# Kernel optimization log

Measured on AMD Instinct MI355X. Metric: run time of the kernel, lower is better.

## Reference

```python
import jax, jax.numpy as jnp
import numpy as np

N, E, H = 100000, 3200000, 128


def setup_inputs() -> dict:
    key = jax.random.key(0)
    ks = jax.random.split(key, 12)
    s = 1.0 / np.sqrt(H)
    x = jax.random.normal(ks[0], (N, H), dtype=jnp.float32)
    edge_index = jax.random.randint(ks[1], (2, E), 0, N, dtype=jnp.int64)
    # GatedGraphConv weight: [num_layers=1, H, H] -> single [H, H]
    W = jax.random.normal(ks[2], (H, H), dtype=jnp.float32) * s
    # GRUCell (gate order: r, z, n)
    gru_w_ih = jax.random.normal(ks[3], (3 * H, H), dtype=jnp.float32) * s
    gru_w_hh = jax.random.normal(ks[4], (3 * H, H), dtype=jnp.float32) * s
    gru_b_ih = jax.random.normal(ks[5], (3 * H,), dtype=jnp.float32) * s
    gru_b_hh = jax.random.normal(ks[6], (3 * H,), dtype=jnp.float32) * s
    # LSTM layer 0 (gate order: i, f, g, o)
    lstm_w_ih = jax.random.normal(ks[7], (4 * H, H), dtype=jnp.float32) * s
    lstm_w_hh = jax.random.normal(ks[8], (4 * H, H), dtype=jnp.float32) * s
    lstm_b_ih = jax.random.normal(ks[9], (4 * H,), dtype=jnp.float32) * s
    lstm_b_hh = jax.random.normal(ks[10], (4 * H,), dtype=jnp.float32) * s
    return {
        "x": x, "edge_index": edge_index, "W": W,
        "gru_w_ih": gru_w_ih, "gru_w_hh": gru_w_hh,
        "gru_b_ih": gru_b_ih, "gru_b_hh": gru_b_hh,
        "lstm_w_ih": lstm_w_ih, "lstm_w_hh": lstm_w_hh,
        "lstm_b_ih": lstm_b_ih, "lstm_b_hh": lstm_b_hh,
    }


def _forward(x, edge_index, W, gru_w_ih, gru_w_hh, gru_b_ih, gru_b_hh,
             lstm_w_ih, lstm_w_hh, lstm_b_ih, lstm_b_hh):
    n = x.shape[0]
    src, dst = edge_index[0], edge_index[1]
    # GatedGraphConv, num_layers=1, mean aggregation
    m = x @ W                                   # [N, H]
    msg = m[src]                                # [E, H] gather (memory-bound)
    agg_sum = jax.ops.segment_sum(msg, dst, num_segments=n)
    deg = jax.ops.segment_sum(jnp.ones((src.shape[0],), x.dtype), dst, num_segments=n)
    agg = agg_sum / jnp.maximum(deg, 1.0)[:, None]
    # GRUCell(agg, x): gates r, z, n
    gi = agg @ gru_w_ih.T + gru_b_ih
    gh = x @ gru_w_hh.T + gru_b_hh
    i_r, i_z, i_n = jnp.split(gi, 3, axis=-1)
    h_r, h_z, h_n = jnp.split(gh, 3, axis=-1)
    r = jax.nn.sigmoid(i_r + h_r)
    z = jax.nn.sigmoid(i_z + h_z)
    ng = jnp.tanh(i_n + r * h_n)
    h_conv = (1.0 - z) * ng + z * x             # conv output H_tilde
    # 1-layer LSTM over seq_len=1 with zero initial (H, C)
    gates = h_conv @ lstm_w_ih.T + lstm_b_ih + lstm_b_hh  # h0 = 0
    i_g, f_g, g_g, o_g = jnp.split(gates, 4, axis=-1)
    c = jax.nn.sigmoid(i_g) * jnp.tanh(g_g)
    h_lstm = jax.nn.sigmoid(o_g) * jnp.tanh(c)
    return jax.nn.relu(h_lstm)


def reference(x, edge_index, W, gru_w_ih, gru_w_hh, gru_b_ih, gru_b_hh,
              lstm_w_ih, lstm_w_hh, lstm_b_ih, lstm_b_hh):
    return _forward(x, edge_index, W, gru_w_ih, gru_w_hh, gru_b_ih, gru_b_hh,
                    lstm_w_ih, lstm_w_hh, lstm_b_ih, lstm_b_hh)
```

## Files before the change

### kernel.cpp

```cpp
#include <hip/hip_runtime.h>
#include <math.h>

#define HD 128
#define PB 256
#define SCB 4096

typedef __attribute__((ext_vector_type(8))) short short8;
typedef __attribute__((ext_vector_type(4))) float f32x4;
typedef __attribute__((ext_vector_type(2))) float f32x2;
typedef __attribute__((ext_vector_type(4))) unsigned u32x4;

__device__ __forceinline__ float sigf(float v) { return 1.0f / (1.0f + __expf(-v)); }
__device__ __forceinline__ float tanhf_fast(float v) {
  float e = __expf(2.0f * v);
  return 1.0f - 2.0f / (e + 1.0f);
}

__device__ __forceinline__ unsigned short f2bf(float f) {
  union { float f; unsigned u; } v; v.f = f;
  unsigned r = (v.u + 0x7fffu + ((v.u >> 16) & 1u)) >> 16;
  return (unsigned short)r;
}
__device__ __forceinline__ float bf2f(unsigned short b) {
  union { unsigned u; float f; } v; v.u = ((unsigned)b) << 16;
  return v.f;
}


__global__ __launch_bounds__(256) void bcount_k(const int* __restrict__ ei,
                                                int* __restrict__ bcnt,
                                                int E, int N, int shift, int NB) {
  __shared__ int h[256];
  const int blk = blockIdx.x, tid = threadIdx.x;
  h[tid] = 0;
  __syncthreads();
  int per = (E + PB - 1) / PB;
  int lo = blk * per;
  int hi = (lo + per < E) ? lo + per : E;
  for (int e = lo + tid; e < hi; e += 256) {
    int d = ei[(size_t)E + e];
    if ((unsigned)d >= (unsigned)N) continue;
    atomicAdd(&h[d >> shift], 1);
  }
  __syncthreads();
  if (tid < NB) bcnt[tid * PB + blk] = h[tid];
}

__global__ __launch_bounds__(256) void scan1_k(const int* __restrict__ a,
                                               int* __restrict__ bsums, int total) {
  __shared__ int ts[256];
  int b = blockIdx.x, tid = threadIdx.x;
  int lo = b * SCB + tid * 16;
  int s = 0;
#pragma unroll
  for (int i = 0; i < 16; ++i) {
    int idx = lo + i;
    if (idx < total) s += a[idx];
  }
  ts[tid] = s;
  __syncthreads();
  for (int off = 128; off > 0; off >>= 1) {
    if (tid < off) ts[tid] += ts[tid + off];
    __syncthreads();
  }
  if (tid == 0) bsums[b] = ts[0];
}

__global__ __launch_bounds__(256) void scan2_k(int* __restrict__ bsums, int nb) {
  __shared__ int ts[256];
  int tid = threadIdx.x;
  int v = (tid < nb) ? bsums[tid] : 0;
  ts[tid] = v;
  __syncthreads();
  for (int off = 1; off < 256; off <<= 1) {
    int u = (tid >= off) ? ts[tid - off] : 0;
    __syncthreads();
    ts[tid] += u;
    __syncthreads();
  }
  if (tid < nb) bsums[tid] = ts[tid] - v;
}

__global__ __launch_bounds__(256) void scan3_k(int* __restrict__ a,
                                               const int* __restrict__ bsums,
                                               int total, int nblk) {
  __shared__ int ts[256];
  int b = blockIdx.x, tid = threadIdx.x;
  int lo = b * SCB + tid * 16;
  int pre[16];
  int s = 0;
#pragma unroll
  for (int i = 0; i < 16; ++i) {
    int idx = lo + i;
    int xv = (idx < total) ? a[idx] : 0;
    pre[i] = s;
    s += xv;
  }
  ts[tid] = s;
  __syncthreads();
  for (int off = 1; off < 256; off <<= 1) {
    int u = (tid >= off) ? ts[tid - off] : 0;
    __syncthreads();
    ts[tid] += u;
    __syncthreads();
  }
  int off0 = ts[tid] - s + bsums[b];
#pragma unroll
  for (int i = 0; i < 16; ++i) {
    int idx = lo + i;
    if (idx < total) a[idx] = off0 + pre[i];
  }
  if (b == nblk - 1 && tid == 255) a[total] = off0 + s;
}

__global__ __launch_bounds__(256) void bpart_k(const int* __restrict__ ei,
                                               const int* __restrict__ bstart,
                                               unsigned* __restrict__ ebuf,
                                               int E, int N, int shift, int NB,
                                               int sbits) {
  __shared__ int cur[256];
  const int blk = blockIdx.x, tid = threadIdx.x;
  if (tid < NB) cur[tid] = bstart[tid * PB + blk];
  __syncthreads();
  int per = (E + PB - 1) / PB;
  int lo = blk * per;
  int hi = (lo + per < E) ? lo + per : E;
  const unsigned dmask = (1u << shift) - 1u;
  for (int e = lo + tid; e < hi; e += 256) {
    int s = ei[e];
    int d = ei[(size_t)E + e];
    if ((unsigned)s >= (unsigned)N || (unsigned)d >= (unsigned)N) continue;
    int p = atomicAdd(&cur[d >> shift], 1);
    ebuf[p] = (((unsigned)d & dmask) << sbits) | (unsigned)s;
  }
}

__global__ __launch_bounds__(256) void bfill2_k(const unsigned* __restrict__ ebuf,
                                                const int* __restrict__ bstart,
                                                int* __restrict__ rowstart,
                                                int* __restrict__ csr,
                                                int N, int shift, int NB, int sbits) {
  __shared__ int cnt[2048];
  __shared__ int tsum[256];
  const int b = blockIdx.x, tid = threadIdx.x;
  const int d0 = b << shift;
  int dmax = d0 + (1 << shift);
  if (dmax > N) dmax = N;
  const int nd = dmax - d0;
  const unsigned smask = (1u << sbits) - 1u;
  for (int i = tid; i < nd; i += 256) cnt[i] = 0;
  __syncthreads();
  const int base = bstart[b * PB];
  const int end = bstart[(b + 1) * PB];
  for (int idx = base + tid; idx < end; idx += 256)
    atomicAdd(&cnt[ebuf[idx] >> sbits], 1);
  __syncthreads();
  const int C = (nd + 255) / 256;
  int lo = tid * C;
  int hi = (lo + C < nd) ? lo + C : nd;
  int loc[8];
  int s = 0;
  for (int i = lo; i < hi; ++i) {
    loc[i - lo] = cnt[i];
    s += cnt[i];
  }
  tsum[tid] = s;
  __syncthreads();
  for (int off = 1; off < 256; off <<= 1) {
    int u = (tid >= off) ? tsum[tid - off] : 0;
    __syncthreads();
    tsum[tid] += u;
    __syncthreads();
  }
  int run = tsum[tid] - s + base;
  for (int i = lo; i < hi; ++i) {
    rowstart[d0 + i] = run;
    cnt[i] = run;
    run += loc[i - lo];
  }
  if (b == NB - 1 && tid == 255) rowstart[N] = end;
  __syncthreads();
  for (int idx = base + tid; idx < end; idx += 256) {
    unsigned pk = ebuf[idx];
    int p = atomicAdd(&cnt[pk >> sbits], 1);
    csr[p] = (int)(pk & smask);
  }
}


__global__ __launch_bounds__(256) void convx_k(const float* __restrict__ x,
                                               unsigned short* __restrict__ xb,
                                               unsigned* __restrict__ x8, int n4) {
  int t = blockIdx.x * 256 + threadIdx.x;
  if (t >= n4) return;
  float4 v = reinterpret_cast<const float4*>(x)[t];
  ushort4 o;
  o.x = f2bf(v.x); o.y = f2bf(v.y); o.z = f2bf(v.z); o.w = f2bf(v.w);
  reinterpret_cast<ushort4*>(xb)[t] = o;
  int p8 = 0;
  p8 = __builtin_amdgcn_cvt_pk_fp8_f32(v.x, v.y, p8, false);
  p8 = __builtin_amdgcn_cvt_pk_fp8_f32(v.z, v.w, p8, true);
  x8[t] = (unsigned)p8;
}

__global__ __launch_bounds__(256) void prepw_k(
    const float* __restrict__ gwhh, const float* __restrict__ lwih,
    const float* __restrict__ lbih, const float* __restrict__ lbhh,
    unsigned short* __restrict__ gwhhb, unsigned short* __restrict__ lwb,
    float* __restrict__ lbias) {
  int t = blockIdx.x * 256 + threadIdx.x;
  if (t < 49152) { gwhhb[t] = f2bf(gwhh[t]); return; }
  t -= 49152;
  if (t < 49152) {
    int j = t >> 7, k = t & 127;
    int jm = j < 128 ? j : j + 128;
    lwb[t] = f2bf(lwih[(size_t)jm * 128 + k]);
    return;
  }
  t -= 49152;
  if (t < 384) {
    int jm = t < 128 ? t : t + 128;
    lbias[t] = lbih[jm] + lbhh[jm];
  }
}

__global__ __launch_bounds__(256) void prepbp_k(const float* __restrict__ W,
                                                const float* __restrict__ gwih,
                                                unsigned short* __restrict__ Bpb) {
  int t = blockIdx.x * 256 + threadIdx.x;
  if (t >= 49152) return;
  int j = t >> 7, k = t & 127;
  const float4* wr = reinterpret_cast<const float4*>(W + (size_t)k * 128);
  const float4* gr = reinterpret_cast<const float4*>(gwih + (size_t)j * 128);
  float acc = 0.f;
#pragma unroll
  for (int c = 0; c < 32; ++c) {
    float4 a = wr[c], b = gr[c];
    acc += a.x * b.x + a.y * b.y + a.z * b.z + a.w * b.w;
  }
  Bpb[t] = f2bf(acc);
}

__device__ __forceinline__ void accf8(f32x2* acc, uint4 v) {
  acc[0] += __builtin_amdgcn_cvt_pk_f32_fp8((int)v.x, false);
  acc[1] += __builtin_amdgcn_cvt_pk_f32_fp8((int)v.x, true);
  acc[2] += __builtin_amdgcn_cvt_pk_f32_fp8((int)v.y, false);
  acc[3] += __builtin_amdgcn_cvt_pk_f32_fp8((int)v.y, true);
  acc[4] += __builtin_amdgcn_cvt_pk_f32_fp8((int)v.z, false);
  acc[5] += __builtin_amdgcn_cvt_pk_f32_fp8((int)v.z, true);
  acc[6] += __builtin_amdgcn_cvt_pk_f32_fp8((int)v.w, false);
  acc[7] += __builtin_amdgcn_cvt_pk_f32_fp8((int)v.w, true);
}

__global__ __launch_bounds__(256) void gather_f8_k(const int* __restrict__ csr,
                                                   const int* __restrict__ rowstart,
                                                   const unsigned* __restrict__ x8,
                                                   unsigned short* __restrict__ xaggb, int N) {
  int w = (int)(((long long)blockIdx.x * 256 + threadIdx.x) >> 6);
  if (w >= N) return;
  const int lane = threadIdx.x & 63;
  const int sub = lane >> 3, li = lane & 7;
  const int beg = rowstart[w], end = rowstart[w + 1];
  const uint4* x4 = reinterpret_cast<const uint4*>(x8);

  f32x2 acc[8];
#pragma unroll
  for (int i = 0; i < 8; ++i) acc[i] = (f32x2)0.f;

  int j = beg;
  for (; j + 32 <= end; j += 32) {
    int s0 = __builtin_nontemporal_load(&csr[j + sub]);
    int s1 = __builtin_nontemporal_load(&csr[j + 8 + sub]);
    int s2 = __builtin_nontemporal_load(&csr[j + 16 + sub]);
    int s3 = __builtin_nontemporal_load(&csr[j + 24 + sub]);
    uint4 v0 = x4[(size_t)s0 * 8 + li];
    uint4 v1 = x4[(size_t)s1 * 8 + li];
    uint4 v2 = x4[(size_t)s2 * 8 + li];
    uint4 v3 = x4[(size_t)s3 * 8 + li];
    accf8(acc, v0);
    accf8(acc, v1);
    accf8(acc, v2);
    accf8(acc, v3);
  }
  for (; j + 8 <= end; j += 8) {
    int s0 = __builtin_nontemporal_load(&csr[j + sub]);
    uint4 v0 = x4[(size_t)s0 * 8 + li];
    accf8(acc, v0);
  }
  int rem = end - j;
  if (sub < rem) {
    int s0 = csr[j + sub];
    uint4 v0 = x4[(size_t)s0 * 8 + li];
    accf8(acc, v0);
  }

  float a16[16];
#pragma unroll
  for (int i = 0; i < 8; ++i) { a16[2 * i] = acc[i].x; a16[2 * i + 1] = acc[i].y; }
#pragma unroll
  for (int i = 0; i < 16; ++i) {
    a16[i] += __shfl_xor(a16[i], 8, 64);
    a16[i] += __shfl_xor(a16[i], 16, 64);
    a16[i] += __shfl_xor(a16[i], 32, 64);
  }

  if (lane < 8) {
    float scale = 1.0f / fmaxf((float)(end - beg), 1.0f);
    u32x4 o1, o2;
    o1.x = (unsigned)f2bf(a16[0] * scale) | ((unsigned)f2bf(a16[1] * scale) << 16);
    o1.y = (unsigned)f2bf(a16[2] * scale) | ((unsigned)f2bf(a16[3] * scale) << 16);
    o1.z = (unsigned)f2bf(a16[4] * scale) | ((unsigned)f2bf(a16[5] * scale) << 16);
    o1.w = (unsigned)f2bf(a16[6] * scale) | ((unsigned)f2bf(a16[7] * scale) << 16);
    o2.x = (unsigned)f2bf(a16[8] * scale) | ((unsigned)f2bf(a16[9] * scale) << 16);
    o2.y = (unsigned)f2bf(a16[10] * scale) | ((unsigned)f2bf(a16[11] * scale) << 16);
    o2.z = (unsigned)f2bf(a16[12] * scale) | ((unsigned)f2bf(a16[13] * scale) << 16);
    o2.w = (unsigned)f2bf(a16[14] * scale) | ((unsigned)f2bf(a16[15] * scale) << 16);
    u32x4* dst = reinterpret_cast<u32x4*>(xaggb + (size_t)w * HD) + li * 2;
    __builtin_nontemporal_store(o1, dst);
    __builtin_nontemporal_store(o2, dst + 1);
  }
}

__global__ __launch_bounds__(256) void gru_fused_k(
    const unsigned short* __restrict__ xaggb, const unsigned short* __restrict__ xb,
    const unsigned short* __restrict__ Bpb, const unsigned short* __restrict__ gwhhb,
    const float* __restrict__ gbih, const float* __restrict__ gbhh,
    unsigned short* __restrict__ hconv, int nrows) {
  __shared__ unsigned short Bsm[6][32][136];
  const int tid = threadIdx.x;
  const int w = tid >> 6, lane = tid & 63;
  const int q = lane >> 4, r = lane & 15;
  const int row0 = blockIdx.y * 64;
  const int c0 = blockIdx.x * 32;

#pragma unroll
  for (int it = 0; it < 12; ++it) {
    int idx = it * 256 + tid;
    int p = idx >> 9;
    int rem = idx & 511;
    int col = rem >> 4, kq = rem & 15;
    const unsigned short* src =
        (p < 3) ? Bpb + ((size_t)(p * 128 + c0 + col)) * HD
                : gwhhb + ((size_t)((p - 3) * 128 + c0 + col)) * HD;
    uint4 v = *reinterpret_cast<const uint4*>(src + kq * 8);
    *reinterpret_cast<uint4*>(&Bsm[p][col][kq * 8]) = v;
  }
  __syncthreads();

  int arow = row0 + (w << 4) + r;
  int ar = arow < nrows ? arow : nrows - 1;
  const unsigned short* Aa = xaggb + (size_t)ar * HD + q * 8;
  const unsigned short* Ax = xb + (size_t)ar * HD + q * 8;

  f32x4 acc[6][2];
#pragma unroll
  for (int p = 0; p < 6; ++p)
#pragma unroll
    for (int cb = 0; cb < 2; ++cb) acc[p][cb] = (f32x4)0.f;

#pragma unroll
  for (int ks = 0; ks < 4; ++ks) {
    short8 a1 = *reinterpret_cast<const short8*>(Aa + ks * 32);
    short8 a2 = *reinterpret_cast<const short8*>(Ax + ks * 32);
#pragma unroll
    for (int p = 0; p < 6; ++p) {
      short8 af = (p < 3) ? a1 : a2;
#pragma unroll
      for (int cb = 0; cb < 2; ++cb) {
        short8 bf = *reinterpret_cast<const short8*>(&Bsm[p][cb * 16 + r][ks * 32 + q * 8]);
        acc[p][cb] = __builtin_amdgcn_mfma_f32_16x16x32_bf16(af, bf, acc[p][cb], 0, 0, 0);
      }
    }
  }

#pragma unroll
  for (int cb = 0; cb < 2; ++cb) {
    int col = c0 + cb * 16 + r;
    float bir = gbih[col], biz = gbih[col + 128], bin = gbih[col + 256];
    float bhr = gbhh[col], bhz = gbhh[col + 128], bhn = gbhh[col + 256];
#pragma unroll
    for (int reg = 0; reg < 4; ++reg) {
      int row = row0 + (w << 4) + q * 4 + reg;
      if (row < nrows) {
        float ir = acc[0][cb][reg] + bir, iz = acc[1][cb][reg] + biz;
        float inn = acc[2][cb][reg] + bin;
        float hr = acc[3][cb][reg] + bhr, hz = acc[4][cb][reg] + bhz;
        float hn = acc[5][cb][reg] + bhn;
        float rr = sigf(ir + hr), zz = sigf(iz + hz);
        float nn = tanhf_fast(inn + rr * hn);
        float xv = bf2f(xb[(size_t)row * HD + col]);
        hconv[(size_t)row * HD + col] = f2bf((1.f - zz) * nn + zz * xv);
      }
    }
  }
}

__global__ __launch_bounds__(256) void lstm_fused_k(
    const unsigned short* __restrict__ hconv, const unsigned short* __restrict__ lwb,
    const float* __restrict__ lbias, float* __restrict__ out, int nrows) {
  __shared__ unsigned short Bsm[3][64][136];
  const int tid = threadIdx.x;
  const int w = tid >> 6, lane = tid & 63;
  const int q = lane >> 4, r = lane & 15;
  const int row0 = blockIdx.y * 64;
  const int c0 = blockIdx.x * 64;

#pragma unroll
  for (int it = 0; it < 12; ++it) {
    int idx = it * 256 + tid;
    int p = idx >> 10, rem = idx & 1023;
    int col = rem >> 4, kq = rem & 15;
    uint4 v = *reinterpret_cast<const uint4*>(
        lwb + ((size_t)(p * 128 + c0 + col)) * HD + kq * 8);
    *reinterpret_cast<uint4*>(&Bsm[p][col][kq * 8]) = v;
  }
  __syncthreads();

  int arow = row0 + (w << 4) + r;
  int ar = arow < nrows ? arow : nrows - 1;
  const unsigned short* Ap = hconv + (size_t)ar * HD + q * 8;

  f32x4 acc[3][4];
#pragma unroll
  for (int p = 0; p < 3; ++p)
#pragma unroll
    for (int cb = 0; cb < 4; ++cb) acc[p][cb] = (f32x4)0.f;

#pragma unroll
  for (int ks = 0; ks < 4; ++ks) {
    short8 af = *reinterpret_cast<const short8*>(Ap + ks * 32);
#pragma unroll
    for (int p = 0; p < 3; ++p)
#pragma unroll
      for (int cb = 0; cb < 4; ++cb) {
        short8 bf = *reinterpret_cast<const short8*>(&Bsm[p][cb * 16 + r][ks * 32 + q * 8]);
        acc[p][cb] = __builtin_amdgcn_mfma_f32_16x16x32_bf16(af, bf, acc[p][cb], 0, 0, 0);
      }
  }

#pragma unroll
  for (int cb = 0; cb < 4; ++cb) {
    int col = c0 + cb * 16 + r;
    float bi = lbias[col], bg = lbias[col + 128], bo = lbias[col + 256];
#pragma unroll
    for (int reg = 0; reg < 4; ++reg) {
      int row = row0 + (w << 4) + q * 4 + reg;
      if (row < nrows) {
        float ig = acc[0][cb][reg] + bi;
        float gg = acc[1][cb][reg] + bg;
        float og = acc[2][cb][reg] + bo;
        float cc = sigf(ig) * tanhf_fast(gg);
        out[(size_t)row * HD + col] = fmaxf(sigf(og) * tanhf_fast(cc), 0.f);
      }
    }
  }
}


extern "C" void kernel_launch(void* const* d_in, const int* in_sizes, int n_in,
                              void* d_out, int out_size, void* d_ws, size_t ws_size,
                              hipStream_t stream) {
  const float* x = (const float*)d_in[0];
  const int* ei = (const int*)d_in[1];
  const float* W = (const float*)d_in[2];
  const float* gw_ih = (const float*)d_in[3];
  const float* gw_hh = (const float*)d_in[4];
  const float* gb_ih = (const float*)d_in[5];
  const float* gb_hh = (const float*)d_in[6];
  const float* lw_ih = (const float*)d_in[7];
  const float* lb_ih = (const float*)d_in[9];
  const float* lb_hh = (const float*)d_in[10];
  float* out = (float*)d_out;

  const int N = in_sizes[0] / HD;
  const int E = in_sizes[1] / 2;
  const size_t nH = (size_t)N * HD;

  int shift = 9;
  while (((N + (1 << shift) - 1) >> shift) > 256) ++shift;
  const int NB = (N + (1 << shift) - 1) >> shift;
  const int sbits = 32 - shift;

  const size_t N4p = (size_t)((N + 1 + 7) & ~7);
  const size_t E4 = (size_t)((E + 3) & ~3);
  const size_t BC = (size_t)NB * PB + 8;
  const int sc_total = NB * PB;
  const int sc_nblk = (sc_total + SCB - 1) / SCB;

  char* p = (char*)d_ws;
  int* rowstart = (int*)p;  p += 4 * N4p;
  int* bcnt = (int*)p;      p += 4 * BC;
  int* bsums = (int*)p;     p += 4 * 64;
  int* csr = (int*)p;       p += 4 * E4;
  size_t sz_eb = 4 * E4, sz_xb = 2 * nH;
  unsigned* ebuf = (unsigned*)p;
  unsigned short* xb = (unsigned short*)p;
  p += (sz_eb > sz_xb ? sz_eb : sz_xb);
  unsigned short* hconv = (unsigned short*)p;  p += 2 * nH;
  unsigned short* Bpb = (unsigned short*)p;    p += 2 * 49152;
  unsigned short* gwhhb = (unsigned short*)p;  p += 2 * 49152;
  unsigned short* lwb = (unsigned short*)p;    p += 2 * 49152;
  float* lbias = (float*)p;                    p += 4 * 384;

  unsigned* x8 = (unsigned*)hconv;

  unsigned short* xaggb = (unsigned short*)d_out;

  dim3 blk(256);
  unsigned rb = (unsigned)((N + 63) / 64);

  bcount_k<<<PB, blk, 0, stream>>>(ei, bcnt, E, N, shift, NB);
  scan1_k<<<sc_nblk, blk, 0, stream>>>(bcnt, bsums, sc_total);
  scan2_k<<<1, blk, 0, stream>>>(bsums, sc_nblk);
  scan3_k<<<sc_nblk, blk, 0, stream>>>(bcnt, bsums, sc_total, sc_nblk);
  bpart_k<<<PB, blk, 0, stream>>>(ei, bcnt, ebuf, E, N, shift, NB, sbits);
  bfill2_k<<<NB, blk, 0, stream>>>(ebuf, bcnt, rowstart, csr, N, shift, NB, sbits);

  convx_k<<<(unsigned)((nH / 4 + 255) / 256), blk, 0, stream>>>(x, xb, x8, (int)(nH / 4));
  prepw_k<<<(2 * 49152 + 384 + 255) / 256, blk, 0, stream>>>(
      gw_hh, lw_ih, lb_ih, lb_hh, gwhhb, lwb, lbias);
  prepbp_k<<<192, blk, 0, stream>>>(W, gw_ih, Bpb);

  long long gthreads = (long long)N * 64;
  gather_f8_k<<<(unsigned)((gthreads + 255) / 256), blk, 0, stream>>>(
      csr, rowstart, x8, xaggb, N);

  gru_fused_k<<<dim3(4, rb), blk, 0, stream>>>(
      xaggb, xb, Bpb, gwhhb, gb_ih, gb_hh, hconv, N);

  lstm_fused_k<<<dim3(2, rb), blk, 0, stream>>>(hconv, lwb, lbias, out, N);
}
```

Baseline: 467.3 us.

## Merge prep kernels, shrink gather unroll, loop column groups inside GRU/LSTM blocks

Fuses the three preprocessing kernels into one launch. The gather inner loop unroll drops from 32 to 16 edges per iteration. The GRU and LSTM kernels now give each block all output columns of a 64-row tile, so A fragments are loaded once and weights are restaged through a smaller shared buffer across four column groups. This trades fewer blocks and repeated A reads for extra barriers and serialized weight staging per block.

```diff
diff --git a/kernel.cpp b/kernel.cpp
--- a/kernel.cpp
+++ b/kernel.cpp
@@ -187,28 +187,28 @@
   }
 }
 
-
-__global__ __launch_bounds__(256) void convx_k(const float* __restrict__ x,
-                                               unsigned short* __restrict__ xb,
-                                               unsigned* __restrict__ x8, int n4) {
-  int t = blockIdx.x * 256 + threadIdx.x;
-  if (t >= n4) return;
-  float4 v = reinterpret_cast<const float4*>(x)[t];
-  ushort4 o;
-  o.x = f2bf(v.x); o.y = f2bf(v.y); o.z = f2bf(v.z); o.w = f2bf(v.w);
-  reinterpret_cast<ushort4*>(xb)[t] = o;
-  int p8 = 0;
-  p8 = __builtin_amdgcn_cvt_pk_fp8_f32(v.x, v.y, p8, false);
-  p8 = __builtin_amdgcn_cvt_pk_fp8_f32(v.z, v.w, p8, true);
-  x8[t] = (unsigned)p8;
-}
-
-__global__ __launch_bounds__(256) void prepw_k(
+__global__ __launch_bounds__(256) void prep_k(
+    const float* __restrict__ x, unsigned short* __restrict__ xb,
+    unsigned* __restrict__ x8,
     const float* __restrict__ gwhh, const float* __restrict__ lwih,
     const float* __restrict__ lbih, const float* __restrict__ lbhh,
     unsigned short* __restrict__ gwhhb, unsigned short* __restrict__ lwb,
-    float* __restrict__ lbias) {
+    float* __restrict__ lbias,
+    const float* __restrict__ W, const float* __restrict__ gwih,
+    unsigned short* __restrict__ Bpb, int n4) {
   int t = blockIdx.x * 256 + threadIdx.x;
+  if (t < n4) {
+    float4 v = reinterpret_cast<const float4*>(x)[t];
+    ushort4 o;
+    o.x = f2bf(v.x); o.y = f2bf(v.y); o.z = f2bf(v.z); o.w = f2bf(v.w);
+    reinterpret_cast<ushort4*>(xb)[t] = o;
+    int p8 = 0;
+    p8 = __builtin_amdgcn_cvt_pk_fp8_f32(v.x, v.y, p8, false);
+    p8 = __builtin_amdgcn_cvt_pk_fp8_f32(v.z, v.w, p8, true);
+    x8[t] = (unsigned)p8;
+    return;
+  }
+  t -= n4;
   if (t < 49152) { gwhhb[t] = f2bf(gwhh[t]); return; }
   t -= 49152;
   if (t < 49152) {
@@ -221,24 +221,21 @@
   if (t < 384) {
     int jm = t < 128 ? t : t + 128;
     lbias[t] = lbih[jm] + lbhh[jm];
-  }
-}
-
-__global__ __launch_bounds__(256) void prepbp_k(const float* __restrict__ W,
-                                                const float* __restrict__ gwih,
-                                                unsigned short* __restrict__ Bpb) {
-  int t = blockIdx.x * 256 + threadIdx.x;
-  if (t >= 49152) return;
-  int j = t >> 7, k = t & 127;
-  const float4* wr = reinterpret_cast<const float4*>(W + (size_t)k * 128);
-  const float4* gr = reinterpret_cast<const float4*>(gwih + (size_t)j * 128);
-  float acc = 0.f;
-#pragma unroll
-  for (int c = 0; c < 32; ++c) {
-    float4 a = wr[c], b = gr[c];
-    acc += a.x * b.x + a.y * b.y + a.z * b.z + a.w * b.w;
-  }
-  Bpb[t] = f2bf(acc);
+    return;
+  }
+  t -= 384;
+  if (t < 49152) {
+    int j = t >> 7, k = t & 127;
+    const float4* wr = reinterpret_cast<const float4*>(W + (size_t)k * 128);
+    const float4* gr = reinterpret_cast<const float4*>(gwih + (size_t)j * 128);
+    float acc = 0.f;
+#pragma unroll
+    for (int c = 0; c < 32; ++c) {
+      float4 a = wr[c], b = gr[c];
+      acc += a.x * b.x + a.y * b.y + a.z * b.z + a.w * b.w;
+    }
+    Bpb[t] = f2bf(acc);
+  }
 }
 
 __device__ __forceinline__ void accf8(f32x2* acc, uint4 v) {
@@ -268,19 +265,13 @@
   for (int i = 0; i < 8; ++i) acc[i] = (f32x2)0.f;
 
   int j = beg;
-  for (; j + 32 <= end; j += 32) {
+  for (; j + 16 <= end; j += 16) {
     int s0 = __builtin_nontemporal_load(&csr[j + sub]);
     int s1 = __builtin_nontemporal_load(&csr[j + 8 + sub]);
-    int s2 = __builtin_nontemporal_load(&csr[j + 16 + sub]);
-    int s3 = __builtin_nontemporal_load(&csr[j + 24 + sub]);
     uint4 v0 = x4[(size_t)s0 * 8 + li];
     uint4 v1 = x4[(size_t)s1 * 8 + li];
-    uint4 v2 = x4[(size_t)s2 * 8 + li];
-    uint4 v3 = x4[(size_t)s3 * 8 + li];
     accf8(acc, v0);
     accf8(acc, v1);
-    accf8(acc, v2);
-    accf8(acc, v3);
   }
   for (; j + 8 <= end; j += 8) {
     int s0 = __builtin_nontemporal_load(&csr[j + sub]);
@@ -326,133 +317,161 @@
     const unsigned short* __restrict__ Bpb, const unsigned short* __restrict__ gwhhb,
     const float* __restrict__ gbih, const float* __restrict__ gbhh,
     unsigned short* __restrict__ hconv, int nrows) {
-  __shared__ unsigned short Bsm[6][32][136];
+  __shared__ unsigned short Bsm[96][136];
   const int tid = threadIdx.x;
   const int w = tid >> 6, lane = tid & 63;
   const int q = lane >> 4, r = lane & 15;
-  const int row0 = blockIdx.y * 64;
-  const int c0 = blockIdx.x * 32;
-
-#pragma unroll
-  for (int it = 0; it < 12; ++it) {
-    int idx = it * 256 + tid;
-    int p = idx >> 9;
-    int rem = idx & 511;
-    int col = rem >> 4, kq = rem & 15;
-    const unsigned short* src =
-        (p < 3) ? Bpb + ((size_t)(p * 128 + c0 + col)) * HD
-                : gwhhb + ((size_t)((p - 3) * 128 + c0 + col)) * HD;
-    uint4 v = *reinterpret_cast<const uint4*>(src + kq * 8);
-    *reinterpret_cast<uint4*>(&Bsm[p][col][kq * 8]) = v;
-  }
-  __syncthreads();
+  const int row0 = blockIdx.x * 64;
 
   int arow = row0 + (w << 4) + r;
   int ar = arow < nrows ? arow : nrows - 1;
   const unsigned short* Aa = xaggb + (size_t)ar * HD + q * 8;
   const unsigned short* Ax = xb + (size_t)ar * HD + q * 8;
-
-  f32x4 acc[6][2];
-#pragma unroll
-  for (int p = 0; p < 6; ++p)
-#pragma unroll
-    for (int cb = 0; cb < 2; ++cb) acc[p][cb] = (f32x4)0.f;
-
+  short8 a1[4], a2[4];
 #pragma unroll
   for (int ks = 0; ks < 4; ++ks) {
-    short8 a1 = *reinterpret_cast<const short8*>(Aa + ks * 32);
-    short8 a2 = *reinterpret_cast<const short8*>(Ax + ks * 32);
-#pragma unroll
-    for (int p = 0; p < 6; ++p) {
-      short8 af = (p < 3) ? a1 : a2;
-#pragma unroll
-      for (int cb = 0; cb < 2; ++cb) {
-        short8 bf = *reinterpret_cast<const short8*>(&Bsm[p][cb * 16 + r][ks * 32 + q * 8]);
-        acc[p][cb] = __builtin_amdgcn_mfma_f32_16x16x32_bf16(af, bf, acc[p][cb], 0, 0, 0);
+    a1[ks] = *reinterpret_cast<const short8*>(Aa + ks * 32);
+    a2[ks] = *reinterpret_cast<const short8*>(Ax + ks * 32);
+  }
+
+  for (int cg = 0; cg < 4; ++cg) {
+    const int c0 = cg * 32;
+    f32x4 acc[6][2];
+#pragma unroll
+    for (int p = 0; p < 6; ++p)
+#pragma unroll
+      for (int cb = 0; cb < 2; ++cb) acc[p][cb] = (f32x4)0.f;
+
+#pragma unroll
+    for (int it = 0; it < 6; ++it) {
+      int idx = it * 256 + tid;
+      int p = idx >> 9, rem = idx & 511;
+      int col = rem >> 4, kq = rem & 15;
+      uint4 v = *reinterpret_cast<const uint4*>(
+          Bpb + ((size_t)(p * 128 + c0 + col)) * HD + kq * 8);
+      *reinterpret_cast<uint4*>(&Bsm[(p << 5) + col][kq * 8]) = v;
+    }
+    __syncthreads();
+#pragma unroll
+    for (int ks = 0; ks < 4; ++ks)
+#pragma unroll
+      for (int p = 0; p < 3; ++p)
+#pragma unroll
+        for (int cb = 0; cb < 2; ++cb) {
+          short8 bf = *reinterpret_cast<const short8*>(
+              &Bsm[(p << 5) + cb * 16 + r][ks * 32 + q * 8]);
+          acc[p][cb] = __builtin_amdgcn_mfma_f32_16x16x32_bf16(a1[ks], bf, acc[p][cb], 0, 0, 0);
+        }
+    __syncthreads();
+
+#pragma unroll
+    for (int it = 0; it < 6; ++it) {
+      int idx = it * 256 + tid;
+      int p = idx >> 9, rem = idx & 511;
+      int col = rem >> 4, kq = rem & 15;
+      uint4 v = *reinterpret_cast<const uint4*>(
+          gwhhb + ((size_t)(p * 128 + c0 + col)) * HD + kq * 8);
+      *reinterpret_cast<uint4*>(&Bsm[(p << 5) + col][kq * 8]) = v;
+    }
+    __syncthreads();
+#pragma unroll
+    for (int ks = 0; ks < 4; ++ks)
+#pragma unroll
+      for (int p = 0; p < 3; ++p)
+#pragma unroll
+        for (int cb = 0; cb < 2; ++cb) {
+          short8 bf = *reinterpret_cast<const short8*>(
+              &Bsm[(p << 5) + cb * 16 + r][ks * 32 + q * 8]);
+          acc[3 + p][cb] = __builtin_amdgcn_mfma_f32_16x16x32_bf16(a2[ks], bf, acc[3 + p][cb], 0, 0, 0);
+        }
+
+#pragma unroll
+    for (int cb = 0; cb < 2; ++cb) {
+      int col = c0 + cb * 16 + r;
+      float bir = gbih[col], biz = gbih[col + 128], bin = gbih[col + 256];
+      float bhr = gbhh[col], bhz = gbhh[col + 128], bhn = gbhh[col + 256];
+#pragma unroll
+      for (int reg = 0; reg < 4; ++reg) {
+        int row = row0 + (w << 4) + q * 4 + reg;
+        if (row < nrows) {
+          float ir = acc[0][cb][reg] + bir, iz = acc[1][cb][reg] + biz;
+          float inn = acc[2][cb][reg] + bin;
+          float hr = acc[3][cb][reg] + bhr, hz = acc[4][cb][reg] + bhz;
+          float hn = acc[5][cb][reg] + bhn;
+          float rr = sigf(ir + hr), zz = sigf(iz + hz);
+          float nn = tanhf_fast(inn + rr * hn);
+          float xv = bf2f(xb[(size_t)row * HD + col]);
+          hconv[(size_t)row * HD + col] = f2bf((1.f - zz) * nn + zz * xv);
+        }
       }
     }
-  }
-
-#pragma unroll
-  for (int cb = 0; cb < 2; ++cb) {
-    int col = c0 + cb * 16 + r;
-    float bir = gbih[col], biz = gbih[col + 128], bin = gbih[col + 256];
-    float bhr = gbhh[col], bhz = gbhh[col + 128], bhn = gbhh[col + 256];
-#pragma unroll
-    for (int reg = 0; reg < 4; ++reg) {
-      int row = row0 + (w << 4) + q * 4 + reg;
-      if (row < nrows) {
-        float ir = acc[0][cb][reg] + bir, iz = acc[1][cb][reg] + biz;
-        float inn = acc[2][cb][reg] + bin;
-        float hr = acc[3][cb][reg] + bhr, hz = acc[4][cb][reg] + bhz;
-        float hn = acc[5][cb][reg] + bhn;
-        float rr = sigf(ir + hr), zz = sigf(iz + hz);
-        float nn = tanhf_fast(inn + rr * hn);
-        float xv = bf2f(xb[(size_t)row * HD + col]);
-        hconv[(size_t)row * HD + col] = f2bf((1.f - zz) * nn + zz * xv);
-      }
-    }
+    __syncthreads();
   }
 }
 
 __global__ __launch_bounds__(256) void lstm_fused_k(
     const unsigned short* __restrict__ hconv, const unsigned short* __restrict__ lwb,
     const float* __restrict__ lbias, float* __restrict__ out, int nrows) {
-  __shared__ unsigned short Bsm[3][64][136];
+  __shared__ unsigned short Bsm[96][136];
   const int tid = threadIdx.x;
   const int w = tid >> 6, lane = tid & 63;
   const int q = lane >> 4, r = lane & 15;
-  const int row0 = blockIdx.y * 64;
-  const int c0 = blockIdx.x * 64;
-
-#pragma unroll
-  for (int it = 0; it < 12; ++it) {
-    int idx = it * 256 + tid;
-    int p = idx >> 10, rem = idx & 1023;
-    int col = rem >> 4, kq = rem & 15;
-    uint4 v = *reinterpret_cast<const uint4*>(
-        lwb + ((size_t)(p * 128 + c0 + col)) * HD + kq * 8);
-    *reinterpret_cast<uint4*>(&Bsm[p][col][kq * 8]) = v;
-  }
-  __syncthreads();
+  const int row0 = blockIdx.x * 64;
 
   int arow = row0 + (w << 4) + r;
   int ar = arow < nrows ? arow : nrows - 1;
   const unsigned short* Ap = hconv + (size_t)ar * HD + q * 8;
-
-  f32x4 acc[3][4];
-#pragma unroll
-  for (int p = 0; p < 3; ++p)
-#pragma unroll
-    for (int cb = 0; cb < 4; ++cb) acc[p][cb] = (f32x4)0.f;
-
-#pragma unroll
-  for (int ks = 0; ks < 4; ++ks) {
-    short8 af = *reinterpret_cast<const short8*>(Ap + ks * 32);
+  short8 hp[4];
+#pragma unroll
+  for (int ks = 0; ks < 4; ++ks)
+    hp[ks] = *reinterpret_cast<const short8*>(Ap + ks * 32);
+
+  for (int cg = 0; cg < 4; ++cg) {
+    const int c0 = cg * 32;
+    f32x4 acc[3][2];
 #pragma unroll
     for (int p = 0; p < 3; ++p)
 #pragma unroll
-      for (int cb = 0; cb < 4; ++cb) {
-        short8 bf = *reinterpret_cast<const short8*>(&Bsm[p][cb * 16 + r][ks * 32 + q * 8]);
-        acc[p][cb] = __builtin_amdgcn_mfma_f32_16x16x32_bf16(af, bf, acc[p][cb], 0, 0, 0);
-      }
-  }
-
-#pragma unroll
-  for (int cb = 0; cb < 4; ++cb) {
-    int col = c0 + cb * 16 + r;
-    float bi = lbias[col], bg = lbias[col + 128], bo = lbias[col + 256];
-#pragma unroll
-    for (int reg = 0; reg < 4; ++reg) {
-      int row = row0 + (w << 4) + q * 4 + reg;
-      if (row < nrows) {
-        float ig = acc[0][cb][reg] + bi;
-        float gg = acc[1][cb][reg] + bg;
-        float og = acc[2][cb][reg] + bo;
-        float cc = sigf(ig) * tanhf_fast(gg);
-        out[(size_t)row * HD + col] = fmaxf(sigf(og) * tanhf_fast(cc), 0.f);
+      for (int cb = 0; cb < 2; ++cb) acc[p][cb] = (f32x4)0.f;
+
+#pragma unroll
+    for (int it = 0; it < 6; ++it) {
+      int idx = it * 256 + tid;
+      int p = idx >> 9, rem = idx & 511;
+      int col = rem >> 4, kq = rem & 15;
+      uint4 v = *reinterpret_cast<const uint4*>(
+          lwb + ((size_t)(p * 128 + c0 + col)) * HD + kq * 8);
+      *reinterpret_cast<uint4*>(&Bsm[(p << 5) + col][kq * 8]) = v;
+    }
+    __syncthreads();
+#pragma unroll
+    for (int ks = 0; ks < 4; ++ks)
+#pragma unroll
+      for (int p = 0; p < 3; ++p)
+#pragma unroll
+        for (int cb = 0; cb < 2; ++cb) {
+          short8 bf = *reinterpret_cast<const short8*>(
+              &Bsm[(p << 5) + cb * 16 + r][ks * 32 + q * 8]);
+          acc[p][cb] = __builtin_amdgcn_mfma_f32_16x16x32_bf16(hp[ks], bf, acc[p][cb], 0, 0, 0);
+        }
+
+#pragma unroll
+    for (int cb = 0; cb < 2; ++cb) {
+      int col = c0 + cb * 16 + r;
+      float bi = lbias[col], bg = lbias[col + 128], bo = lbias[col + 256];
+#pragma unroll
+      for (int reg = 0; reg < 4; ++reg) {
+        int row = row0 + (w << 4) + q * 4 + reg;
+        if (row < nrows) {
+          float ig = acc[0][cb][reg] + bi;
+          float gg = acc[1][cb][reg] + bg;
+          float og = acc[2][cb][reg] + bo;
+          float cc = sigf(ig) * tanhf_fast(gg);
+          out[(size_t)row * HD + col] = fmaxf(sigf(og) * tanhf_fast(cc), 0.f);
+        }
       }
     }
+    __syncthreads();
   }
 }
 
@@ -516,17 +535,17 @@
   bpart_k<<<PB, blk, 0, stream>>>(ei, bcnt, ebuf, E, N, shift, NB, sbits);
   bfill2_k<<<NB, blk, 0, stream>>>(ebuf, bcnt, rowstart, csr, N, shift, NB, sbits);
 
-  convx_k<<<(unsigned)((nH / 4 + 255) / 256), blk, 0, stream>>>(x, xb, x8, (int)(nH / 4));
-  prepw_k<<<(2 * 49152 + 384 + 255) / 256, blk, 0, stream>>>(
-      gw_hh, lw_ih, lb_ih, lb_hh, gwhhb, lwb, lbias);
-  prepbp_k<<<192, blk, 0, stream>>>(W, gw_ih, Bpb);
+  int n4 = (int)(nH / 4);
+  int prep_total = n4 + 49152 + 49152 + 384 + 49152;
+  prep_k<<<(unsigned)((prep_total + 255) / 256), blk, 0, stream>>>(
+      x, xb, x8, gw_hh, lw_ih, lb_ih, lb_hh, gwhhb, lwb, lbias, W, gw_ih, Bpb, n4);
 
   long long gthreads = (long long)N * 64;
   gather_f8_k<<<(unsigned)((gthreads + 255) / 256), blk, 0, stream>>>(
       csr, rowstart, x8, xaggb, N);
 
-  gru_fused_k<<<dim3(4, rb), blk, 0, stream>>>(
+  gru_fused_k<<<rb, blk, 0, stream>>>(
       xaggb, xb, Bpb, gwhhb, gb_ih, gb_hh, hconv, N);
 
-  lstm_fused_k<<<dim3(2, rb), blk, 0, stream>>>(hconv, lwb, lbias, out, N);
-}
+  lstm_fused_k<<<rb, blk, 0, stream>>>(hconv, lwb, lbias, out, N);
+}
```

Result: no change. 471.2 us (+0.8%).
